# Performance work log

Hardware: AMD Instinct MI355X
Metric: run time of the kernel (lower is better)

## Reference

```python
import jax, jax.numpy as jnp
import numpy as np

KH, KW = 3, 3
STRIDE = (1, 1)


def setup_inputs() -> dict:
    key = jax.random.key(0)
    k1, k2, k3 = jax.random.split(key, 3)
    N, C, H, W = 16, 128, 64, 64
    O = 128
    x = jax.random.normal(k1, (N, C, H, W), dtype=jnp.float32)
    # Flat weight layout [O, C*KH*KW], matching torch reshape of [O,C,KH,KW]
    weight = jax.random.normal(k2, (O, C * KH * KW), dtype=jnp.float32) * 0.02
    bias = jax.random.normal(k3, (O, 1), dtype=jnp.float32) * 0.02
    return {"x": x, "weight": weight, "bias": bias}


def reference(x, weight, bias):
    O = weight.shape[0]
    C = x.shape[1]
    # [O, C*KH*KW] -> [O, C, KH, KW]; flattening order (C major, then kh, kw)
    # matches the module's unfold/permute im2col layout.
    w4 = weight.reshape(O, C, KH, KW)
    out = jax.lax.conv_general_dilated(
        x, w4,
        window_strides=STRIDE,
        padding='VALID',
        dimension_numbers=('NCHW', 'OIHW', 'NCHW'),
    )
    return out + bias.reshape(1, O, 1, 1)
```

## Files before the change

### kernel.cpp

```cpp
#include <hip/hip_runtime.h>
#include <stdint.h>

#define AS_G __attribute__((address_space(1)))
#define AS_L __attribute__((address_space(3)))

typedef __bf16 bf16x8 __attribute__((ext_vector_type(8)));
typedef float  f32x4  __attribute__((ext_vector_type(4)));

static constexpr int NIMG = 16, CIN = 128, H = 64, W = 64, OCH = 128;
static constexpr int HO = 62, WO = 62;
static constexpr int PIX = HO * WO;
static constexpr int M_TOT = NIMG * PIX;
static constexpr int K_TOT = CIN * 9;
static constexpr int BM = 256, BK = 64;
static constexpr int KSTEPS = K_TOT / BK;
static constexpr int NWG = (M_TOT + BM - 1) / BM;
static constexpr int ASZ = BM * BK * 2;
static constexpr int BSZ = OCH * BK * 2;
static constexpr int SLOT = ASZ + BSZ;
static constexpr int LDS_BYTES = 3 * SLOT;

__device__ __forceinline__ unsigned short f2bf(float f) {
    union { float f; uint32_t u; } v; v.f = f;
    uint32_t u = v.u;
    return (unsigned short)((u + 0x7FFFu + ((u >> 16) & 1u)) >> 16);
}

__global__ __launch_bounds__(256) void prep_kernel(const float* __restrict__ x,
                                                   const float* __restrict__ wsrc,
                                                   unsigned short* __restrict__ xt,
                                                   unsigned short* __restrict__ bpd) {
    __shared__ float lds[CIN][W + 4];
    if (blockIdx.x < NIMG * H) {
        const int n   = blockIdx.x >> 6;
        const int h   = blockIdx.x & 63;
        const int tid = threadIdx.x;
        {
            const int c  = tid >> 1;
            const int w0 = (tid & 1) * 32;
            const float* src = x + (((size_t)(n * CIN + c) * H + h) * W + w0);
            #pragma unroll
            for (int j = 0; j < 8; ++j) {
                float4 v = *reinterpret_cast<const float4*>(src + j * 4);
                *reinterpret_cast<float4*>(&lds[c][w0 + j * 4]) = v;
            }
        }
        __syncthreads();
        {
            const int w  = tid >> 2;
            const int c0 = (tid & 3) * 32;
            unsigned short* dst = xt + (((size_t)(n * H + h) * W + w) * CIN + c0);
            uint32_t pk[16];
            #pragma unroll
            for (int j = 0; j < 16; ++j) {
                uint32_t lo = f2bf(lds[c0 + 2 * j][w]);
                uint32_t hi = f2bf(lds[c0 + 2 * j + 1][w]);
                pk[j] = lo | (hi << 16);
            }
            #pragma unroll
            for (int j = 0; j < 4; ++j) {
                *reinterpret_cast<uint4*>(dst + j * 8) =
                    make_uint4(pk[4 * j], pk[4 * j + 1], pk[4 * j + 2], pk[4 * j + 3]);
            }
        }
    } else {
        int tid = (blockIdx.x - NIMG * H) * 256 + threadIdx.x;
        if (tid < OCH * K_TOT) {
            int o  = tid / K_TOT;
            int kp = tid - o * K_TOT;
            int t  = kp >> 7;
            int c  = kp & 127;
            bpd[tid] = f2bf(wsrc[o * K_TOT + c * 9 + t]);
        }
    }
}

__global__ __launch_bounds__(512, 1) void gemm_kernel(const unsigned short* __restrict__ xt,
                                                      const unsigned short* __restrict__ bp,
                                                      const float* __restrict__ bias,
                                                      float* __restrict__ out) {
    extern __shared__ char lds[];
    const int tid  = threadIdx.x;
    const int wv   = tid >> 6;
    const int lane = tid & 63;

    const int orig = blockIdx.x;
    const int xcd  = orig & 7;
    const int idx  = orig >> 3;
    const int wg   = (xcd == 0 ? 0 : 31 + (xcd - 1) * 30) + idx;
    const int m0   = wg * BM;

    const int csel = ((tid & 7) ^ ((tid >> 3) & 7)) * 8;
    int aBase[4];
    #pragma unroll
    for (int p = 0; p < 4; ++p) {
        int row = p * 64 + (tid >> 3);
        int m = m0 + row; if (m >= M_TOT) m = M_TOT - 1;
        int n  = m / PIX;
        int r  = m - n * PIX;
        int y  = r / WO;
        int xx = r - y * WO;
        aBase[p] = ((n * H + y) * W + xx) * CIN;
    }
    int bBase[2];
    #pragma unroll
    for (int p = 0; p < 2; ++p)
        bBase[p] = (p * 64 + (tid >> 3)) * K_TOT;

    auto stage = [&](char* dst, int step) {
        const int t  = step >> 1;
        const int c0 = (step & 1) * 64;
        const int tapoff = (t / 3) * (W * CIN) + (t % 3) * CIN + c0;
        const int kb = step * BK;
        #pragma unroll
        for (int p = 0; p < 4; ++p)
            __builtin_amdgcn_global_load_lds(
                (AS_G unsigned int*)(xt + aBase[p] + tapoff + csel),
                (AS_L unsigned int*)(dst + p * 8192 + wv * 1024), 16, 0, 0);
        #pragma unroll
        for (int p = 0; p < 2; ++p)
            __builtin_amdgcn_global_load_lds(
                (AS_G unsigned int*)(bp + bBase[p] + kb + csel),
                (AS_L unsigned int*)(dst + ASZ + p * 8192 + wv * 1024), 16, 0, 0);
    };

    const int wr = wv >> 1, wc = wv & 1;
    const int lr = lane & 15, lq = lane >> 4;
    const int aRow = (wr * 64 + lr) * 128;
    const int bRow = ASZ + (wc * 64 + lr) * 128;
    int colx[2];
    #pragma unroll
    for (int ks = 0; ks < 2; ++ks)
        colx[ks] = (ks * 64 + lq * 16) ^ ((lane & 7) << 4);

    f32x4 acc[4][4];
    #pragma unroll
    for (int a = 0; a < 4; ++a)
        #pragma unroll
        for (int b = 0; b < 4; ++b)
            acc[a][b] = (f32x4){0.f, 0.f, 0.f, 0.f};

    auto compute = [&](const char* base) {
        #pragma unroll
        for (int ks = 0; ks < 2; ++ks) {
            bf16x8 af[4], bfr[4];
            #pragma unroll
            for (int mi = 0; mi < 4; ++mi)
                af[mi] = *(const bf16x8*)(base + aRow + mi * 2048 + colx[ks]);
            #pragma unroll
            for (int ni = 0; ni < 4; ++ni)
                bfr[ni] = *(const bf16x8*)(base + bRow + ni * 2048 + colx[ks]);
            __builtin_amdgcn_s_setprio(1);
            #pragma unroll
            for (int mi = 0; mi < 4; ++mi)
                #pragma unroll
                for (int ni = 0; ni < 4; ++ni)
                    acc[mi][ni] = __builtin_amdgcn_mfma_f32_16x16x32_bf16(
                        bfr[ni], af[mi], acc[mi][ni], 0, 0, 0);
            __builtin_amdgcn_s_setprio(0);
        }
    };

    char* b0 = lds;
    char* b1 = lds + SLOT;
    char* b2 = lds + 2 * SLOT;
    stage(b0, 0);
    stage(b1, 1);
    for (int t = 0; t < KSTEPS - 2; ++t) {
        stage(b2, t + 2);
        asm volatile("s_waitcnt vmcnt(12)" ::: "memory");
        __builtin_amdgcn_s_barrier();
        __builtin_amdgcn_sched_barrier(0);
        compute(b0);
        asm volatile("s_waitcnt lgkmcnt(0)" ::: "memory");
        __builtin_amdgcn_s_barrier();
        __builtin_amdgcn_sched_barrier(0);
        char* tmp = b0; b0 = b1; b1 = b2; b2 = tmp;
    }
    asm volatile("s_waitcnt vmcnt(6)" ::: "memory");
    __builtin_amdgcn_s_barrier();
    __builtin_amdgcn_sched_barrier(0);
    compute(b0);
    asm volatile("s_waitcnt vmcnt(0)" ::: "memory");
    __builtin_amdgcn_s_barrier();
    __builtin_amdgcn_sched_barrier(0);
    compute(b1);

    f32x4 bv[4];
    #pragma unroll
    for (int ni = 0; ni < 4; ++ni)
        bv[ni] = *(const f32x4*)(bias + wc * 64 + ni * 16 + lq * 4);
    #pragma unroll
    for (int mi = 0; mi < 4; ++mi) {
        int m = m0 + wr * 64 + mi * 16 + lr;
        if (m < M_TOT) {
            int n  = m / PIX;
            int r  = m - n * PIX;
            int y  = r / WO;
            int xx = r - y * WO;
            float* ob = out + (size_t)n * OCH * PIX + y * WO + xx;
            #pragma unroll
            for (int ni = 0; ni < 4; ++ni)
                #pragma unroll
                for (int j = 0; j < 4; ++j) {
                    int o = wc * 64 + ni * 16 + lq * 4 + j;
                    ob[(size_t)o * PIX] = acc[mi][ni][j] + bv[ni][j];
                }
        }
    }
}

extern "C" void kernel_launch(void* const* d_in, const int* in_sizes, int n_in,
                              void* d_out, int out_size, void* d_ws, size_t ws_size,
                              hipStream_t stream) {
    const float* x    = (const float*)d_in[0];
    const float* wsrc = (const float*)d_in[1];
    const float* bias = (const float*)d_in[2];
    float* out = (float*)d_out;
    unsigned short* xt = (unsigned short*)d_ws;
    unsigned short* bp = xt + (size_t)NIMG * H * W * CIN;
    prep_kernel<<<dim3(NIMG * H + (OCH * K_TOT + 255) / 256), dim3(256), 0, stream>>>(
        x, wsrc, xt, bp);
    gemm_kernel<<<dim3(NWG), dim3(512), LDS_BYTES, stream>>>(xt, bp, bias, out);
}
```

Baseline: 47.70 us.

## Interleave global-to-LDS staging with per-k-substep MFMA compute in main loop

Restructures the triple-buffered main loop so the next stage's global-to-LDS loads are split across the two k-substeps and issued after each substep's LDS fragment reads, with barriers placed between the reads and the MFMA block. Waits on vmcnt move to the end of each iteration, and the prologue and epilogue special cases fold into one loop driven by a doStage predicate. The aim is to spread memory issue across the compute phases and overlap it better with the matrix instructions. In exchange the loop has more barriers per iteration, which adds synchronisation cost.

```diff
diff --git a/kernel.cpp b/kernel.cpp
--- a/kernel.cpp
+++ b/kernel.cpp
@@ -13,7 +13,7 @@
 static constexpr int M_TOT = NIMG * PIX;
 static constexpr int K_TOT = CIN * 9;
 static constexpr int BM = 256, BK = 64;
-static constexpr int KSTEPS = K_TOT / BK;
+static constexpr int NT = K_TOT / BK;
 static constexpr int NWG = (M_TOT + BM - 1) / BM;
 static constexpr int ASZ = BM * BK * 2;
 static constexpr int BSZ = OCH * BK * 2;
@@ -107,21 +107,17 @@
     for (int p = 0; p < 2; ++p)
         bBase[p] = (p * 64 + (tid >> 3)) * K_TOT;
 
-    auto stage = [&](char* dst, int step) {
-        const int t  = step >> 1;
-        const int c0 = (step & 1) * 64;
-        const int tapoff = (t / 3) * (W * CIN) + (t % 3) * CIN + c0;
-        const int kb = step * BK;
-        #pragma unroll
-        for (int p = 0; p < 4; ++p)
-            __builtin_amdgcn_global_load_lds(
-                (AS_G unsigned int*)(xt + aBase[p] + tapoff + csel),
-                (AS_L unsigned int*)(dst + p * 8192 + wv * 1024), 16, 0, 0);
-        #pragma unroll
-        for (int p = 0; p < 2; ++p)
-            __builtin_amdgcn_global_load_lds(
-                (AS_G unsigned int*)(bp + bBase[p] + kb + csel),
-                (AS_L unsigned int*)(dst + ASZ + p * 8192 + wv * 1024), 16, 0, 0);
+    auto stA = [&](char* dst, int step, int p) {
+        const int tt = step >> 1, c0 = (step & 1) * 64;
+        const int tapoff = (tt / 3) * (W * CIN) + (tt % 3) * CIN + c0;
+        __builtin_amdgcn_global_load_lds(
+            (AS_G unsigned int*)(xt + aBase[p] + tapoff + csel),
+            (AS_L unsigned int*)(dst + p * 8192 + wv * 1024), 16, 0, 0);
+    };
+    auto stB = [&](char* dst, int step, int p) {
+        __builtin_amdgcn_global_load_lds(
+            (AS_G unsigned int*)(bp + bBase[p] + step * BK + csel),
+            (AS_L unsigned int*)(dst + ASZ + p * 8192 + wv * 1024), 16, 0, 0);
     };
 
     const int wr = wv >> 1, wc = wv & 1;
@@ -140,16 +136,37 @@
         for (int b = 0; b < 4; ++b)
             acc[a][b] = (f32x4){0.f, 0.f, 0.f, 0.f};
 
-    auto compute = [&](const char* base) {
+    {
+        char* d0 = lds;
+        char* d1 = lds + SLOT;
         #pragma unroll
-        for (int ks = 0; ks < 2; ++ks) {
+        for (int p = 0; p < 4; ++p) stA(d0, 0, p);
+        stB(d0, 0, 0); stB(d0, 0, 1);
+        #pragma unroll
+        for (int p = 0; p < 4; ++p) stA(d1, 1, p);
+        stB(d1, 1, 0); stB(d1, 1, 1);
+        asm volatile("s_waitcnt vmcnt(6)" ::: "memory");
+        __builtin_amdgcn_s_barrier();
+        __builtin_amdgcn_sched_barrier(0);
+    }
+
+    for (int t = 0; t < NT; ++t) {
+        const char* cur = lds + (t % 3) * SLOT;
+        char* nxt = lds + ((t + 2) % 3) * SLOT;
+        const bool doStage = (t + 2 < NT);
+        const int st = t + 2;
+        {
             bf16x8 af[4], bfr[4];
             #pragma unroll
             for (int mi = 0; mi < 4; ++mi)
-                af[mi] = *(const bf16x8*)(base + aRow + mi * 2048 + colx[ks]);
+                af[mi] = *(const bf16x8*)(cur + aRow + mi * 2048 + colx[0]);
             #pragma unroll
             for (int ni = 0; ni < 4; ++ni)
-                bfr[ni] = *(const bf16x8*)(base + bRow + ni * 2048 + colx[ks]);
+                bfr[ni] = *(const bf16x8*)(cur + bRow + ni * 2048 + colx[0]);
+            if (doStage) { stA(nxt, st, 0); stA(nxt, st, 1); stA(nxt, st, 2); }
+            __builtin_amdgcn_s_barrier();
+            asm volatile("s_waitcnt lgkmcnt(0)" ::: "memory");
+            __builtin_amdgcn_sched_barrier(0);
             __builtin_amdgcn_s_setprio(1);
             #pragma unroll
             for (int mi = 0; mi < 4; ++mi)
@@ -158,33 +175,34 @@
                     acc[mi][ni] = __builtin_amdgcn_mfma_f32_16x16x32_bf16(
                         bfr[ni], af[mi], acc[mi][ni], 0, 0, 0);
             __builtin_amdgcn_s_setprio(0);
-        }
-    };
-
-    char* b0 = lds;
-    char* b1 = lds + SLOT;
-    char* b2 = lds + 2 * SLOT;
-    stage(b0, 0);
-    stage(b1, 1);
-    for (int t = 0; t < KSTEPS - 2; ++t) {
-        stage(b2, t + 2);
-        asm volatile("s_waitcnt vmcnt(12)" ::: "memory");
-        __builtin_amdgcn_s_barrier();
-        __builtin_amdgcn_sched_barrier(0);
-        compute(b0);
-        asm volatile("s_waitcnt lgkmcnt(0)" ::: "memory");
-        __builtin_amdgcn_s_barrier();
-        __builtin_amdgcn_sched_barrier(0);
-        char* tmp = b0; b0 = b1; b1 = b2; b2 = tmp;
-    }
-    asm volatile("s_waitcnt vmcnt(6)" ::: "memory");
-    __builtin_amdgcn_s_barrier();
-    __builtin_amdgcn_sched_barrier(0);
-    compute(b0);
-    asm volatile("s_waitcnt vmcnt(0)" ::: "memory");
-    __builtin_amdgcn_s_barrier();
-    __builtin_amdgcn_sched_barrier(0);
-    compute(b1);
+            __builtin_amdgcn_s_barrier();
+        }
+        {
+            bf16x8 af[4], bfr[4];
+            #pragma unroll
+            for (int mi = 0; mi < 4; ++mi)
+                af[mi] = *(const bf16x8*)(cur + aRow + mi * 2048 + colx[1]);
+            #pragma unroll
+            for (int ni = 0; ni < 4; ++ni)
+                bfr[ni] = *(const bf16x8*)(cur + bRow + ni * 2048 + colx[1]);
+            if (doStage) { stA(nxt, st, 3); stB(nxt, st, 0); stB(nxt, st, 1); }
+            __builtin_amdgcn_s_barrier();
+            asm volatile("s_waitcnt lgkmcnt(0)" ::: "memory");
+            __builtin_amdgcn_sched_barrier(0);
+            __builtin_amdgcn_s_setprio(1);
+            #pragma unroll
+            for (int mi = 0; mi < 4; ++mi)
+                #pragma unroll
+                for (int ni = 0; ni < 4; ++ni)
+                    acc[mi][ni] = __builtin_amdgcn_mfma_f32_16x16x32_bf16(
+                        bfr[ni], af[mi], acc[mi][ni], 0, 0, 0);
+            __builtin_amdgcn_s_setprio(0);
+            if (t < NT - 2)      asm volatile("s_waitcnt vmcnt(6)" ::: "memory");
+            else if (t < NT - 1) asm volatile("s_waitcnt vmcnt(0)" ::: "memory");
+            __builtin_amdgcn_s_barrier();
+            __builtin_amdgcn_sched_barrier(0);
+        }
+    }
 
     f32x4 bv[4];
     #pragma unroll
```

New measurement: 46.11 us. -3.3%, faster.
